# Performance work log

Hardware: AMD Instinct MI355X
Metric: run time of the kernel (lower is better)

## Reference

```python
import jax, jax.numpy as jnp
import numpy as np

N_NODES = 25000
N_EDGES = 500000
ND, ED, G = 32, 19, 200


def _lrelu(x):
    return jax.nn.leaky_relu(x, 0.01)


def setup_inputs() -> dict:
    key = jax.random.key(0)
    ks = jax.random.split(key, 12)
    s = 0.05
    return {
        "node_feats": jax.random.normal(ks[0], (N_NODES, ND), jnp.float32),
        "edge_feats": jax.random.normal(ks[1], (N_EDGES, ED), jnp.float32),
        "src": jax.random.randint(ks[2], (N_EDGES,), 0, N_NODES),
        "dst": jax.random.randint(ks[3], (N_EDGES,), 0, N_NODES),
        "Wn": jax.random.normal(ks[4], (G, ND), jnp.float32) * s,
        "bn": jnp.zeros((G,), jnp.float32),
        "We1": jax.random.normal(ks[5], (G, ND + ED), jnp.float32) * s,
        "be1": jnp.zeros((G,), jnp.float32),
        "We2": jax.random.normal(ks[6], (1, 2 * G), jnp.float32) * s,
        "be2": jnp.zeros((1,), jnp.float32),
        "Wet": jax.random.normal(ks[7], (G, G), jnp.float32) * s,
        "bet": jnp.zeros((G,), jnp.float32),
        "W_ih": jax.random.normal(ks[8], (3 * G, G), jnp.float32) * s,
        "b_ih": jnp.zeros((3 * G,), jnp.float32),
        "W_hh": jax.random.normal(ks[9], (3 * G, G), jnp.float32) * s,
        "b_hh": jnp.zeros((3 * G,), jnp.float32),
    }


def reference(node_feats, edge_feats, src, dst, Wn, bn, We1, be1, We2, be2,
              Wet, bet, W_ih, b_ih, W_hh, b_hh):
    N = node_feats.shape[0]
    # project_node: Linear + LeakyReLU -> hv_new [N, G]
    hv_new = _lrelu(node_feats @ Wn.T + bn)
    # apply_edges1 + project_edge1: cat([src hv, he]) -> he1 [E, G]
    he1 = _lrelu(jnp.concatenate([node_feats[src], edge_feats], axis=1) @ We1.T + be1)
    # apply_edges2 + project_edge2: cat([dst hv_new, he1]) -> logits [E, 1]
    he2 = jnp.concatenate([hv_new[dst], he1], axis=1)
    logits = _lrelu(he2 @ We2.T + be2)[:, 0]  # [E]
    # edge_softmax: softmax over incoming edges per destination node
    m = jax.ops.segment_max(logits, dst, num_segments=N)  # [N]
    ex = jnp.exp(logits - m[dst])
    denom = jax.ops.segment_sum(ex, dst, num_segments=N)  # [N]
    a = ex / denom[dst]  # [E]
    # AttentiveGRU1: e = a * edge_transform(he1); scatter-sum to dst
    e = a[:, None] * (he1 @ Wet.T + bet)  # [E, G]
    c = jax.ops.segment_sum(e, dst, num_segments=N)  # [N, G]
    context = jax.nn.elu(c)
    # GRUCell(context, hv_new)
    gi = context @ W_ih.T + b_ih
    gh = hv_new @ W_hh.T + b_hh
    ir, iz, inn = jnp.split(gi, 3, axis=1)
    hr, hz, hn = jnp.split(gh, 3, axis=1)
    r = jax.nn.sigmoid(ir + hr)
    z = jax.nn.sigmoid(iz + hz)
    n = jnp.tanh(inn + r * hn)
    h = (1.0 - z) * n + z * hv_new
    return jax.nn.relu(h)
```

## Files before the change

### kernel.cpp

```cpp
#include <hip/hip_runtime.h>
#include <hip/hip_bf16.h>

#define G 200
#define NDIM 32
#define EDIM 19
#define KIN 51

typedef unsigned short u16;
typedef unsigned int u32;
typedef unsigned long long u64;

typedef __attribute__((ext_vector_type(8))) short bfrag;
typedef __attribute__((ext_vector_type(4))) float ffrag;

__device__ __forceinline__ float lrelu(float x){ return x > 0.f ? x : 0.01f*x; }
__device__ __forceinline__ u16 f2b(float x){ u32 u = __float_as_uint(x); return (u16)((u + 0x7fffu + ((u >> 16) & 1u)) >> 16); }
__device__ __forceinline__ float b2f(u16 x){ return __uint_as_float(((u32)x) << 16); }

#define MFMA16(a, b, c) __builtin_amdgcn_mfma_f32_16x16x32_bf16(a, b, c, 0, 0, 0)

__global__ void zero_kernel(float* __restrict__ s_raw, float* __restrict__ denom,
                            int* __restrict__ deg, float* __restrict__ l1, int N){
  int i = blockIdx.x * 256 + threadIdx.x;
  if (i < N * G) s_raw[i] = 0.f;
  if (i < N){ denom[i] = 0.f; deg[i] = 0; l1[i] = 0.f; }
}

__global__ void prep_all_kernel(const float* __restrict__ We1, const float* __restrict__ Wn,
                                const float* __restrict__ Wet, const float* __restrict__ Wih,
                                const float* __restrict__ Whh,
                                u16* __restrict__ Wbg, u16* __restrict__ Wnb, u16* __restrict__ Wet2,
                                u16* __restrict__ Wrz, u16* __restrict__ Winn, u16* __restrict__ Whn){
  int idx = blockIdx.x * 256 + threadIdx.x;
  const int s0 = 208 * 64, s1 = 256 * 64, s2 = 208 * 224, s3 = 2 * 208 * 416, s4 = 208 * 224, s5 = 208 * 224;
  if (idx < s0){
    int r = idx >> 6, k = idx & 63;
    Wbg[idx] = f2b((r < G && k < KIN) ? We1[r * KIN + k] : 0.f);
    return;
  }
  idx -= s0;
  if (idx < s1){
    int r = idx >> 6, k = idx & 63;
    Wnb[idx] = f2b((r < G && k < NDIM) ? Wn[r * NDIM + k] : 0.f);
    return;
  }
  idx -= s1;
  if (idx < s2){
    int r = idx / 224, k = idx % 224;
    Wet2[idx] = f2b((r < G && k < G) ? Wet[r * G + k] : 0.f);
    return;
  }
  idx -= s2;
  if (idx < s3){
    int g = idx / (208 * 416), rem = idx % (208 * 416);
    int r = rem / 416, k = rem % 416;
    float v = 0.f;
    if (r < G){
      int row = g * G + r;
      if (k < G) v = Wih[row * G + k];
      else if (k >= 208 && k < 408) v = Whh[row * G + (k - 208)];
    }
    Wrz[idx] = f2b(v);
    return;
  }
  idx -= s3;
  if (idx < s4){
    int r = idx / 224, k = idx % 224;
    Winn[idx] = f2b((r < G && k < G) ? Wih[(2 * G + r) * G + k] : 0.f);
    return;
  }
  idx -= s4;
  if (idx < s5){
    int r = idx / 224, kk = idx % 224;
    Whn[idx] = f2b((r < G && kk >= 16 && kk < 216) ? Whh[(2 * G + r) * G + (kk - 16)] : 0.f);
  }
}

__global__ void deghist_kernel(const int* __restrict__ dst, int* __restrict__ deg, int E){
  int e = blockIdx.x * 256 + threadIdx.x;
  if (e < E) atomicAdd(&deg[dst[e]], 1);
}

__global__ __launch_bounds__(1024) void scan_kernel(const int* __restrict__ deg, int* __restrict__ offs,
                                                    int* __restrict__ cur, int N){
  __shared__ int wsums[16];
  __shared__ int carry_s;
  int tid = threadIdx.x;
  int lane = tid & 63, wid = tid >> 6;
  if (tid == 0) carry_s = 0;
  __syncthreads();
  for (int base = 0; base < N; base += 1024){
    int i = base + tid;
    int v = (i < N) ? deg[i] : 0;
    int x = v;
    #pragma unroll
    for (int off = 1; off < 64; off <<= 1){
      int y = __shfl_up(x, off, 64);
      if (lane >= off) x += y;
    }
    if (lane == 63) wsums[wid] = x;
    __syncthreads();
    if (wid == 0){
      int w = (lane < 16) ? wsums[lane] : 0;
      #pragma unroll
      for (int off = 1; off < 16; off <<= 1){
        int y = __shfl_up(w, off, 64);
        if (lane >= off) w += y;
      }
      if (lane < 16) wsums[lane] = w;
    }
    __syncthreads();
    int wexcl = (wid == 0) ? 0 : wsums[wid - 1];
    int incl = carry_s + wexcl + x;
    if (i < N){ offs[i] = incl - v; cur[i] = incl - v; }
    __syncthreads();
    if (tid == 1023) carry_s = incl;
    __syncthreads();
  }
  if (threadIdx.x == 0) offs[N] = carry_s;
}

__global__ void scatter_kernel(const int* __restrict__ dst, const int* __restrict__ src,
                               int* __restrict__ cur, int* __restrict__ eids,
                               int* __restrict__ dstc, int* __restrict__ srcc, int E){
  int e = blockIdx.x * 256 + threadIdx.x;
  if (e < E){
    int d = dst[e];
    int pos = atomicAdd(&cur[d], 1);
    eids[pos] = e;
    dstc[pos] = d;
    srcc[pos] = src[e];
  }
}

__global__ __launch_bounds__(256) void hvgemm_kernel(
    const float* __restrict__ nf, const u16* __restrict__ Wnb, const float* __restrict__ bn,
    const float* __restrict__ We2, float* __restrict__ hv, float* __restrict__ l1, int M)
{
  __shared__ __align__(16) u16 As[64][72];
  __shared__ __align__(16) u16 Ws[64][72];
  int tid = threadIdx.x;
  int m0 = blockIdx.y * 64, n0 = blockIdx.x * 64;
  int l = tid & 63, w = tid >> 6, quad = l >> 4, col = l & 15;

  for (int idx = tid; idx < 64 * 16; idx += 256){
    int r = idx >> 4, c4 = idx & 15;
    int row = m0 + r, k = c4 * 4;
    float4 v = make_float4(0.f,0.f,0.f,0.f);
    if (row < M && k < NDIM) v = *(const float4*)(nf + (long)row * NDIM + k);
    *(ushort4*)&As[r][c4 * 4] = make_ushort4(f2b(v.x), f2b(v.y), f2b(v.z), f2b(v.w));
  }
  for (int idx = tid; idx < 64 * 8; idx += 256){
    int r = idx >> 3, c = idx & 7;
    *(ulonglong2*)&Ws[r][c * 8] = *(const ulonglong2*)(Wnb + (long)(n0 + r) * 64 + c * 8);
  }
  __syncthreads();
  bfrag a0 = *(const bfrag*)&As[w * 16 + col][quad * 8];
  bfrag a1 = *(const bfrag*)&As[w * 16 + col][32 + quad * 8];
  ffrag acc[4];
  #pragma unroll
  for (int t = 0; t < 4; ++t){ acc[t].x = 0.f; acc[t].y = 0.f; acc[t].z = 0.f; acc[t].w = 0.f; }
  #pragma unroll
  for (int t = 0; t < 4; ++t){
    bfrag b0 = *(const bfrag*)&Ws[t * 16 + col][quad * 8];
    bfrag b1 = *(const bfrag*)&Ws[t * 16 + col][32 + quad * 8];
    acc[t] = MFMA16(a0, b0, acc[t]);
    acc[t] = MFMA16(a1, b1, acc[t]);
  }
  float lp[4] = {0.f, 0.f, 0.f, 0.f};
  #pragma unroll
  for (int t = 0; t < 4; ++t){
    int n = n0 + t * 16 + col;
    float bv = (n < G) ? bn[n] : 0.f;
    float wv = (n < G) ? We2[n] : 0.f;
    #pragma unroll
    for (int r = 0; r < 4; ++r){
      int row = m0 + w * 16 + quad * 4 + r;
      float v = lrelu(acc[t][r] + bv);
      lp[r] += wv * v;
      if (n < G && row < M) hv[(long)row * G + n] = v;
    }
  }
  #pragma unroll
  for (int r = 0; r < 4; ++r){
    lp[r] += __shfl_xor(lp[r], 1, 16);
    lp[r] += __shfl_xor(lp[r], 2, 16);
    lp[r] += __shfl_xor(lp[r], 4, 16);
    lp[r] += __shfl_xor(lp[r], 8, 16);
  }
  if (col == 0){
    #pragma unroll
    for (int r = 0; r < 4; ++r){
      int row = m0 + w * 16 + quad * 4 + r;
      if (row < M) atomicAdd(&l1[row], lp[r]);
    }
  }
}

#define SST 72
__global__ __launch_bounds__(256) void edge_csr_kernel(
    const float* __restrict__ nf, const float* __restrict__ ef,
    const int* __restrict__ eids, const int* __restrict__ dstc, const int* __restrict__ srcc,
    const int* __restrict__ offs,
    const u16* __restrict__ Wbg, const float* __restrict__ be1,
    const float* __restrict__ We2, const float* __restrict__ be2,
    const float* __restrict__ l1,
    float* __restrict__ s_raw, float* __restrict__ denom, int E)
{
  __shared__ __align__(16) u16 shm[208 * SST];
  __shared__ u32 bw_s[208];
  __shared__ int node_s[64], es[64], srcs[64], segnode[64];
  __shared__ __align__(16) u16 exb[64];
  __shared__ __align__(8) unsigned char segb[64];
  __shared__ int Svar;

  int tid = threadIdx.x;
  int j0 = blockIdx.x * 64;

  if (tid < 64){
    int j = j0 + tid;
    int valid = j < E;
    int e = valid ? eids[j] : 0;
    es[tid] = e;
    srcs[tid] = valid ? srcc[j] : 0;
    int n = valid ? dstc[j] : -1;
    node_s[tid] = n;
    int nn = (tid == 63 || j + 1 >= E) ? -2 : dstc[j + 1];
    int f1 = (valid && n != nn) ? 1 : 0;
    int f2 = 0;
    if (f1 && offs[n] >= j0 && offs[n + 1] <= j0 + 64) f2 = 1;
    u64 em = __ballot(f1 != 0);
    int seg = (int)__popcll(em & ((1ull << tid) - 1ull));
    segb[tid] = (unsigned char)seg;
    if (f1) segnode[seg] = (n << 1) | f2;
    if (tid == 0) Svar = (int)__popcll(em);
  }
  if (tid < 208){
    float bv = (tid < G) ? be1[tid] : 0.f;
    float wv = (tid < G) ? We2[G + tid] : 0.f;
    bw_s[tid] = (u32)f2b(bv) | ((u32)f2b(wv) << 16);
  }
  __syncthreads();

  for (int idx = tid; idx < 64 * 8; idx += 256){
    int el = idx >> 3, c = idx & 7;
    float4 v = make_float4(0.f,0.f,0.f,0.f);
    if (j0 + el < E) v = *(const float4*)(nf + (long)srcs[el] * NDIM + c * 4);
    *(ushort4*)&shm[el * SST + c * 4] = make_ushort4(f2b(v.x), f2b(v.y), f2b(v.z), f2b(v.w));
  }
  for (int idx = tid; idx < 64 * EDIM; idx += 256){
    int el = idx / EDIM, k = idx - el * EDIM;
    float v = 0.f;
    if (j0 + el < E) v = ef[(long)es[el] * EDIM + k];
    shm[el * SST + NDIM + k] = f2b(v);
  }
  for (int idx = tid; idx < 64 * 13; idx += 256){
    int el = idx / 13, kk = idx - el * 13;
    shm[el * SST + KIN + kk] = 0;
  }
  __syncthreads();

  int l = tid & 63, w = tid >> 6;
  int quad = l >> 4, col = l & 15;
  int m0 = w * 16;

  bfrag a0 = *(const bfrag*)&shm[(m0 + col) * SST + quad * 8];
  bfrag a1 = *(const bfrag*)&shm[(m0 + col) * SST + 32 + quad * 8];
  __syncthreads();

  if (tid < 64) shm[200 * SST + tid] = 0x3F80;

  float pl[4] = {0.f, 0.f, 0.f, 0.f};
  #pragma unroll
  for (int t = 0; t < 13; ++t){
    bfrag b0 = *(const bfrag*)(Wbg + (t * 16 + col) * 64 + quad * 8);
    bfrag b1 = *(const bfrag*)(Wbg + (t * 16 + col) * 64 + 32 + quad * 8);
    ffrag acc; acc.x = 0.f; acc.y = 0.f; acc.z = 0.f; acc.w = 0.f;
    acc = MFMA16(a0, b0, acc);
    acc = MFMA16(a1, b1, acc);
    int g = t * 16 + col;
    u32 bw = bw_s[g];
    float bv = b2f((u16)(bw & 0xFFFF)), wv = b2f((u16)(bw >> 16));
    float v0 = lrelu(acc.x + bv), v1 = lrelu(acc.y + bv);
    float v2 = lrelu(acc.z + bv), v3 = lrelu(acc.w + bv);
    pl[0] += wv * v0; pl[1] += wv * v1; pl[2] += wv * v2; pl[3] += wv * v3;
    if (g < G)
      *(ushort4*)&shm[g * SST + m0 + quad * 4] = make_ushort4(f2b(v0), f2b(v1), f2b(v2), f2b(v3));
  }
  #pragma unroll
  for (int r = 0; r < 4; ++r){
    pl[r] += __shfl_xor(pl[r], 1, 16);
    pl[r] += __shfl_xor(pl[r], 2, 16);
    pl[r] += __shfl_xor(pl[r], 4, 16);
    pl[r] += __shfl_xor(pl[r], 8, 16);
  }
  if (col == 0){
    #pragma unroll
    for (int r = 0; r < 4; ++r){
      int el = m0 + quad * 4 + r;
      float ex = 0.f;
      if (j0 + el < E){
        int n = node_s[el];
        float lg = lrelu(pl[r] + l1[n] + be2[0]);
        ex = __expf(lg);
      }
      exb[el] = f2b(ex);
    }
  }
  __syncthreads();

  int S = Svar;
  for (int mt = 0; mt * 16 < S; ++mt){
    int m = mt * 16 + col;
    u64 sb0 = *(const u64*)&segb[quad * 8];
    u64 sb1 = *(const u64*)&segb[32 + quad * 8];
    ulonglong2 ew0 = *(const ulonglong2*)&exb[quad * 8];
    ulonglong2 ew1 = *(const ulonglong2*)&exb[32 + quad * 8];
    bfrag A0, A1;
    #pragma unroll
    for (int jj = 0; jj < 8; ++jj){
      int s0i = (int)((sb0 >> (8 * jj)) & 0xFF);
      int s1i = (int)((sb1 >> (8 * jj)) & 0xFF);
      u64 w0 = (jj < 4) ? ew0.x : ew0.y;
      u64 w1 = (jj < 4) ? ew1.x : ew1.y;
      u16 e0 = (u16)(w0 >> (16 * (jj & 3)));
      u16 e1 = (u16)(w1 >> (16 * (jj & 3)));
      A0[jj] = (s0i == m) ? (short)e0 : (short)0;
      A1[jj] = (s1i == m) ? (short)e1 : (short)0;
    }
    int cnt = (w == 3) ? 4 : 3;
    for (int i = 0; i < cnt; ++i){
      int t = w * 3 + i;
      bfrag b0 = *(const bfrag*)&shm[(t * 16 + col) * SST + quad * 8];
      bfrag b1 = *(const bfrag*)&shm[(t * 16 + col) * SST + 32 + quad * 8];
      ffrag acc; acc.x = 0.f; acc.y = 0.f; acc.z = 0.f; acc.w = 0.f;
      acc = MFMA16(A0, b0, acc);
      acc = MFMA16(A1, b1, acc);
      int g = t * 16 + col;
      #pragma unroll
      for (int r = 0; r < 4; ++r){
        int seg = mt * 16 + quad * 4 + r;
        if (seg < S && g <= 200){
          int enc = segnode[seg];
          int nd = enc >> 1;
          float v = acc[r];
          float* pd = (g < G) ? (s_raw + (long)nd * G + g) : (denom + nd);
          if (enc & 1) *pd = v; else atomicAdd(pd, v);
        }
      }
    }
  }
}

__global__ __launch_bounds__(256) void ctxgru_kernel(
    const float* __restrict__ s_raw, const float* __restrict__ hv, const float* __restrict__ denom,
    const u16* __restrict__ Wet2, const u16* __restrict__ Wrz,
    const u16* __restrict__ Winn, const u16* __restrict__ Whn,
    const float* __restrict__ bet, const float* __restrict__ b_ih, const float* __restrict__ b_hh,
    float* __restrict__ out, int M)
{
  __shared__ __align__(16) u16 X[64 * 416];
  __shared__ float invds[64];
  int tid = threadIdx.x;
  int m0 = blockIdx.x * 64;

  if (tid < 64){
    float dn = (m0 + tid < M) ? denom[m0 + tid] : 0.f;
    invds[tid] = dn > 0.f ? 1.f / dn : 0.f;
  }
  __syncthreads();

  for (int idx = tid; idx < 64 * 50; idx += 256){
    int r = idx / 50, c = idx % 50;
    int row = m0 + r;
    float4 v = make_float4(0.f,0.f,0.f,0.f), h = make_float4(0.f,0.f,0.f,0.f);
    if (row < M){
      v = *(const float4*)(s_raw + (long)row * G + c * 4);
      h = *(const float4*)(hv + (long)row * G + c * 4);
    }
    float iv = invds[r];
    *(ushort4*)&X[r * 416 + c * 4] = make_ushort4(f2b(v.x*iv), f2b(v.y*iv), f2b(v.z*iv), f2b(v.w*iv));
    *(ushort4*)&X[r * 416 + 208 + c * 4] = make_ushort4(f2b(h.x), f2b(h.y), f2b(h.z), f2b(h.w));
  }
  for (int idx = tid; idx < 64 * 4; idx += 256){
    int r = idx / 4, q = idx % 4;
    int base = (q < 2) ? (200 + q * 4) : (408 + (q - 2) * 4);
    *(ushort4*)&X[r * 416 + base] = make_ushort4(0,0,0,0);
  }
  __syncthreads();

  int l = tid & 63, w = tid >> 6, quad = l >> 4, col = l & 15;
  int rowbase = w * 16;

  bfrag a1[7];
  #pragma unroll
  for (int j = 0; j < 7; ++j) a1[j] = *(const bfrag*)&X[(rowbase + col) * 416 + j * 32 + quad * 8];

  for (int st = 0; st < 13; ++st){
    int n = st * 16 + col;
    ffrag acc; acc.x = 0.f; acc.y = 0.f; acc.z = 0.f; acc.w = 0.f;
    #pragma unroll
    for (int j = 0; j < 7; ++j){
      bfrag b = *(const bfrag*)(Wet2 + (long)n * 224 + j * 32 + quad * 8);
      acc = MFMA16(a1[j], b, acc);
    }
    if (n < G){
      float bv = bet[n];
      #pragma unroll
      for (int r = 0; r < 4; ++r){
        int lr = rowbase + quad * 4 + r;
        float gate = invds[lr] > 0.f ? 1.f : 0.f;
        float v = acc[r] + gate * bv;
        v = (v > 0.f) ? v : (__expf(v) - 1.f);
        X[lr * 416 + n] = f2b(v);
      }
    }
  }
  __syncthreads();

  bfrag a2[13];
  #pragma unroll
  for (int j = 0; j < 13; ++j) a2[j] = *(const bfrag*)&X[(rowbase + col) * 416 + j * 32 + quad * 8];

  for (int st = 0; st < 13; ++st){
    int n = st * 16 + col;
    ffrag ar, az, ai, ah;
    ar.x=ar.y=ar.z=ar.w=0.f; az.x=az.y=az.z=az.w=0.f;
    ai.x=ai.y=ai.z=ai.w=0.f; ah.x=ah.y=ah.z=ah.w=0.f;
    #pragma unroll
    for (int j = 0; j < 13; ++j){
      bfrag br_ = *(const bfrag*)(Wrz + (long)n * 416 + j * 32 + quad * 8);
      ar = MFMA16(a2[j], br_, ar);
      bfrag bz_ = *(const bfrag*)(Wrz + (long)(208 + n) * 416 + j * 32 + quad * 8);
      az = MFMA16(a2[j], bz_, az);
    }
    #pragma unroll
    for (int j = 0; j < 7; ++j){
      bfrag bi_ = *(const bfrag*)(Winn + (long)n * 224 + j * 32 + quad * 8);
      ai = MFMA16(a2[j], bi_, ai);
      bfrag bh_ = *(const bfrag*)(Whn + (long)n * 224 + j * 32 + quad * 8);
      ah = MFMA16(a2[j + 6], bh_, ah);
    }
    if (n < G){
      float br = b_ih[n] + b_hh[n];
      float bz = b_ih[G + n] + b_hh[G + n];
      float bi = b_ih[2 * G + n];
      float bh = b_hh[2 * G + n];
      #pragma unroll
      for (int r = 0; r < 4; ++r){
        int lr = rowbase + quad * 4 + r;
        int row = m0 + lr;
        if (row < M){
          float rg = 1.f / (1.f + __expf(-(ar[r] + br)));
          float zg = 1.f / (1.f + __expf(-(az[r] + bz)));
          float ng = tanhf(ai[r] + bi + rg * (ah[r] + bh));
          float hvv = b2f(X[lr * 416 + 208 + n]);
          float h = (1.f - zg) * ng + zg * hvv;
          out[(long)row * G + n] = h > 0.f ? h : 0.f;
        }
      }
    }
  }
}

extern "C" void kernel_launch(void* const* d_in, const int* in_sizes, int n_in,
                              void* d_out, int out_size, void* d_ws, size_t ws_size,
                              hipStream_t stream)
{
  const float* nf   = (const float*)d_in[0];
  const float* ef   = (const float*)d_in[1];
  const int*   src  = (const int*)d_in[2];
  const int*   dst  = (const int*)d_in[3];
  const float* Wn   = (const float*)d_in[4];
  const float* bn   = (const float*)d_in[5];
  const float* We1  = (const float*)d_in[6];
  const float* be1  = (const float*)d_in[7];
  const float* We2  = (const float*)d_in[8];
  const float* be2  = (const float*)d_in[9];
  const float* Wet  = (const float*)d_in[10];
  const float* bet  = (const float*)d_in[11];
  const float* W_ih = (const float*)d_in[12];
  const float* b_ih = (const float*)d_in[13];
  const float* W_hh = (const float*)d_in[14];
  const float* b_hh = (const float*)d_in[15];
  int N = in_sizes[0] / NDIM;
  int E = in_sizes[2];
  float* out = (float*)d_out;

  char* p = (char*)d_ws;
  auto alloc = [&](size_t b){ char* r = p; p += (b + 255) & ~(size_t)255; return r; };
  float* hv    = (float*)alloc((size_t)N * G * 4);
  float* s_raw = (float*)alloc((size_t)N * G * 4);
  float* denom = (float*)alloc((size_t)N * 4);
  int*   deg   = (int*)  alloc((size_t)N * 4);
  int*   offs  = (int*)  alloc((size_t)(N + 1) * 4);
  int*   cur   = (int*)  alloc((size_t)N * 4);
  int*   eids  = (int*)  alloc((size_t)E * 4);
  int*   dstc  = (int*)  alloc((size_t)E * 4);
  int*   srcc  = (int*)  alloc((size_t)E * 4);
  float* l1    = (float*)alloc((size_t)N * 4);
  u16*   Wbg   = (u16*)  alloc((size_t)208 * 64 * 2);
  u16*   Wnb   = (u16*)  alloc((size_t)256 * 64 * 2);
  u16*   Wet2  = (u16*)  alloc((size_t)208 * 224 * 2);
  u16*   Wrz   = (u16*)  alloc((size_t)2 * 208 * 416 * 2);
  u16*   Winn  = (u16*)  alloc((size_t)208 * 224 * 2);
  u16*   Whn   = (u16*)  alloc((size_t)208 * 224 * 2);

  int eb = (E + 255) / 256;
  int mb = (N + 63) / 64;
  const int prep_total = 208*64 + 256*64 + 208*224 + 2*208*416 + 208*224 + 208*224;

  zero_kernel<<<dim3((N * G + 255) / 256), dim3(256), 0, stream>>>(s_raw, denom, deg, l1, N);
  prep_all_kernel<<<dim3((prep_total + 255) / 256), dim3(256), 0, stream>>>(
      We1, Wn, Wet, W_ih, W_hh, Wbg, Wnb, Wet2, Wrz, Winn, Whn);
  deghist_kernel<<<dim3(eb), dim3(256), 0, stream>>>(dst, deg, E);
  scan_kernel<<<dim3(1), dim3(1024), 0, stream>>>(deg, offs, cur, N);
  scatter_kernel<<<dim3(eb), dim3(256), 0, stream>>>(dst, src, cur, eids, dstc, srcc, E);
  hvgemm_kernel<<<dim3(4, mb), dim3(256), 0, stream>>>(nf, Wnb, bn, We2, hv, l1, N);
  edge_csr_kernel<<<dim3((E + 63) / 64), dim3(256), 0, stream>>>(nf, ef, eids, dstc, srcc, offs,
                                                                 Wbg, be1, We2, be2, l1, s_raw, denom, E);
  ctxgru_kernel<<<dim3(mb), dim3(256), 0, stream>>>(s_raw, hv, denom, Wet2, Wrz, Winn, Whn,
                                                    bet, b_ih, b_hh, out, N);
}
```

Before: 458.8 us.

## Pack edge data in CSR order as bf16, single-pass scan, pad GRU smem stride

After: 435.7 us. 1.05x faster.

```diff
diff --git a/kernel.cpp b/kernel.cpp
--- a/kernel.cpp
+++ b/kernel.cpp
@@ -20,10 +20,12 @@
 #define MFMA16(a, b, c) __builtin_amdgcn_mfma_f32_16x16x32_bf16(a, b, c, 0, 0, 0)
 
 __global__ void zero_kernel(float* __restrict__ s_raw, float* __restrict__ denom,
-                            int* __restrict__ deg, float* __restrict__ l1, int N){
+                            int* __restrict__ deg, float* __restrict__ l1,
+                            const float* __restrict__ nf, u16* __restrict__ nfb, int N){
   int i = blockIdx.x * 256 + threadIdx.x;
   if (i < N * G) s_raw[i] = 0.f;
   if (i < N){ denom[i] = 0.f; deg[i] = 0; l1[i] = 0.f; }
+  if (i < N * NDIM) nfb[i] = f2b(nf[i]);
 }
 
 __global__ void prep_all_kernel(const float* __restrict__ We1, const float* __restrict__ Wn,
@@ -84,53 +86,66 @@
 __global__ __launch_bounds__(1024) void scan_kernel(const int* __restrict__ deg, int* __restrict__ offs,
                                                     int* __restrict__ cur, int N){
   __shared__ int wsums[16];
-  __shared__ int carry_s;
+  const int C = 25;
   int tid = threadIdx.x;
   int lane = tid & 63, wid = tid >> 6;
-  if (tid == 0) carry_s = 0;
-  __syncthreads();
-  for (int base = 0; base < N; base += 1024){
-    int i = base + tid;
-    int v = (i < N) ? deg[i] : 0;
-    int x = v;
-    #pragma unroll
-    for (int off = 1; off < 64; off <<= 1){
-      int y = __shfl_up(x, off, 64);
-      if (lane >= off) x += y;
-    }
-    if (lane == 63) wsums[wid] = x;
-    __syncthreads();
-    if (wid == 0){
-      int w = (lane < 16) ? wsums[lane] : 0;
-      #pragma unroll
-      for (int off = 1; off < 16; off <<= 1){
-        int y = __shfl_up(w, off, 64);
-        if (lane >= off) w += y;
-      }
-      if (lane < 16) wsums[lane] = w;
-    }
-    __syncthreads();
-    int wexcl = (wid == 0) ? 0 : wsums[wid - 1];
-    int incl = carry_s + wexcl + x;
-    if (i < N){ offs[i] = incl - v; cur[i] = incl - v; }
-    __syncthreads();
-    if (tid == 1023) carry_s = incl;
-    __syncthreads();
-  }
-  if (threadIdx.x == 0) offs[N] = carry_s;
-}
-
-__global__ void scatter_kernel(const int* __restrict__ dst, const int* __restrict__ src,
-                               int* __restrict__ cur, int* __restrict__ eids,
-                               int* __restrict__ dstc, int* __restrict__ srcc, int E){
+  int base = tid * C;
+  int loc[C];
+  int s = 0;
+  #pragma unroll
+  for (int i = 0; i < C; ++i){
+    int v = (base + i < N) ? deg[base + i] : 0;
+    loc[i] = s; s += v;
+  }
+  int x = s;
+  #pragma unroll
+  for (int off = 1; off < 64; off <<= 1){
+    int y = __shfl_up(x, off, 64);
+    if (lane >= off) x += y;
+  }
+  if (lane == 63) wsums[wid] = x;
+  __syncthreads();
+  if (wid == 0){
+    int w = (lane < 16) ? wsums[lane] : 0;
+    #pragma unroll
+    for (int off = 1; off < 16; off <<= 1){
+      int y = __shfl_up(w, off, 64);
+      if (lane >= off) w += y;
+    }
+    if (lane < 16) wsums[lane] = w;
+  }
+  __syncthreads();
+  int excl = ((wid ? wsums[wid - 1] : 0) + x) - s;
+  #pragma unroll
+  for (int i = 0; i < C; ++i){
+    int o = excl + loc[i];
+    if (base + i < N){ offs[base + i] = o; cur[base + i] = o; }
+  }
+  if (tid == 1023) offs[N] = excl + s;
+}
+
+__global__ void scatter_pack_kernel(const int* __restrict__ dst, const int* __restrict__ src,
+                                    const float* __restrict__ ef,
+                                    int* __restrict__ cur, int2* __restrict__ ds2,
+                                    u16* __restrict__ efc, int E){
   int e = blockIdx.x * 256 + threadIdx.x;
-  if (e < E){
-    int d = dst[e];
-    int pos = atomicAdd(&cur[d], 1);
-    eids[pos] = e;
-    dstc[pos] = d;
-    srcc[pos] = src[e];
-  }
+  if (e >= E) return;
+  int d = dst[e];
+  int pos = atomicAdd(&cur[d], 1);
+  ds2[pos] = make_int2(d, src[e]);
+  const float* ep = ef + (long)e * EDIM;
+  u32 w[12];
+  #pragma unroll
+  for (int j = 0; j < 12; ++j){
+    int k0 = 2 * j, k1 = 2 * j + 1;
+    u16 lo = (k0 < EDIM) ? f2b(ep[k0]) : (u16)0;
+    u16 hi = (k1 < EDIM) ? f2b(ep[k1]) : (u16)0;
+    w[j] = (u32)lo | ((u32)hi << 16);
+  }
+  uint4* dp = (uint4*)(efc + (long)pos * 24);
+  dp[0] = make_uint4(w[0], w[1], w[2], w[3]);
+  dp[1] = make_uint4(w[4], w[5], w[6], w[7]);
+  dp[2] = make_uint4(w[8], w[9], w[10], w[11]);
 }
 
 __global__ __launch_bounds__(256) void hvgemm_kernel(
@@ -199,9 +214,8 @@
 
 #define SST 72
 __global__ __launch_bounds__(256) void edge_csr_kernel(
-    const float* __restrict__ nf, const float* __restrict__ ef,
-    const int* __restrict__ eids, const int* __restrict__ dstc, const int* __restrict__ srcc,
-    const int* __restrict__ offs,
+    const u16* __restrict__ nfb, const u16* __restrict__ efc,
+    const int2* __restrict__ ds2, const int* __restrict__ offs,
     const u16* __restrict__ Wbg, const float* __restrict__ be1,
     const float* __restrict__ We2, const float* __restrict__ be2,
     const float* __restrict__ l1,
@@ -209,7 +223,7 @@
 {
   __shared__ __align__(16) u16 shm[208 * SST];
   __shared__ u32 bw_s[208];
-  __shared__ int node_s[64], es[64], srcs[64], segnode[64];
+  __shared__ int node_s[64], srcs[64], segnode[64];
   __shared__ __align__(16) u16 exb[64];
   __shared__ __align__(8) unsigned char segb[64];
   __shared__ int Svar;
@@ -220,12 +234,11 @@
   if (tid < 64){
     int j = j0 + tid;
     int valid = j < E;
-    int e = valid ? eids[j] : 0;
-    es[tid] = e;
-    srcs[tid] = valid ? srcc[j] : 0;
-    int n = valid ? dstc[j] : -1;
+    int2 p = valid ? ds2[j] : make_int2(-1, 0);
+    srcs[tid] = p.y;
+    int n = valid ? p.x : -1;
     node_s[tid] = n;
-    int nn = (tid == 63 || j + 1 >= E) ? -2 : dstc[j + 1];
+    int nn = (tid == 63 || j + 1 >= E) ? -2 : ds2[j + 1].x;
     int f1 = (valid && n != nn) ? 1 : 0;
     int f2 = 0;
     if (f1 && offs[n] >= j0 && offs[n + 1] <= j0 + 64) f2 = 1;
@@ -242,22 +255,19 @@
   }
   __syncthreads();
 
-  for (int idx = tid; idx < 64 * 8; idx += 256){
-    int el = idx >> 3, c = idx & 7;
-    float4 v = make_float4(0.f,0.f,0.f,0.f);
-    if (j0 + el < E) v = *(const float4*)(nf + (long)srcs[el] * NDIM + c * 4);
-    *(ushort4*)&shm[el * SST + c * 4] = make_ushort4(f2b(v.x), f2b(v.y), f2b(v.z), f2b(v.w));
-  }
-  for (int idx = tid; idx < 64 * EDIM; idx += 256){
-    int el = idx / EDIM, k = idx - el * EDIM;
-    float v = 0.f;
-    if (j0 + el < E) v = ef[(long)es[el] * EDIM + k];
-    shm[el * SST + NDIM + k] = f2b(v);
-  }
-  for (int idx = tid; idx < 64 * 13; idx += 256){
-    int el = idx / 13, kk = idx - el * 13;
-    shm[el * SST + KIN + kk] = 0;
-  }
+  for (int idx = tid; idx < 64 * 4; idx += 256){
+    int el = idx >> 2, c = idx & 3;
+    ulonglong2 v; v.x = 0; v.y = 0;
+    if (j0 + el < E) v = *(const ulonglong2*)(nfb + (long)srcs[el] * NDIM + c * 8);
+    *(ulonglong2*)&shm[el * SST + c * 8] = v;
+  }
+  for (int idx = tid; idx < 64 * 3; idx += 256){
+    int el = idx / 3, c = idx - el * 3;
+    ulonglong2 v; v.x = 0; v.y = 0;
+    if (j0 + el < E) v = *(const ulonglong2*)(efc + (long)(j0 + el) * 24 + c * 8);
+    *(ulonglong2*)&shm[el * SST + NDIM + c * 8] = v;
+  }
+  if (tid < 64){ ulonglong2 z; z.x = 0; z.y = 0; *(ulonglong2*)&shm[tid * SST + 56] = z; }
   __syncthreads();
 
   int l = tid & 63, w = tid >> 6;
@@ -352,6 +362,7 @@
   }
 }
 
+#define XST 420
 __global__ __launch_bounds__(256) void ctxgru_kernel(
     const float* __restrict__ s_raw, const float* __restrict__ hv, const float* __restrict__ denom,
     const u16* __restrict__ Wet2, const u16* __restrict__ Wrz,
@@ -359,7 +370,7 @@
     const float* __restrict__ bet, const float* __restrict__ b_ih, const float* __restrict__ b_hh,
     float* __restrict__ out, int M)
 {
-  __shared__ __align__(16) u16 X[64 * 416];
+  __shared__ __align__(16) u16 X[64 * XST];
   __shared__ float invds[64];
   int tid = threadIdx.x;
   int m0 = blockIdx.x * 64;
@@ -379,13 +390,13 @@
       h = *(const float4*)(hv + (long)row * G + c * 4);
     }
     float iv = invds[r];
-    *(ushort4*)&X[r * 416 + c * 4] = make_ushort4(f2b(v.x*iv), f2b(v.y*iv), f2b(v.z*iv), f2b(v.w*iv));
-    *(ushort4*)&X[r * 416 + 208 + c * 4] = make_ushort4(f2b(h.x), f2b(h.y), f2b(h.z), f2b(h.w));
+    *(ushort4*)&X[r * XST + c * 4] = make_ushort4(f2b(v.x*iv), f2b(v.y*iv), f2b(v.z*iv), f2b(v.w*iv));
+    *(ushort4*)&X[r * XST + 208 + c * 4] = make_ushort4(f2b(h.x), f2b(h.y), f2b(h.z), f2b(h.w));
   }
   for (int idx = tid; idx < 64 * 4; idx += 256){
     int r = idx / 4, q = idx % 4;
     int base = (q < 2) ? (200 + q * 4) : (408 + (q - 2) * 4);
-    *(ushort4*)&X[r * 416 + base] = make_ushort4(0,0,0,0);
+    *(ushort4*)&X[r * XST + base] = make_ushort4(0,0,0,0);
   }
   __syncthreads();
 
@@ -394,7 +405,7 @@
 
   bfrag a1[7];
   #pragma unroll
-  for (int j = 0; j < 7; ++j) a1[j] = *(const bfrag*)&X[(rowbase + col) * 416 + j * 32 + quad * 8];
+  for (int j = 0; j < 7; ++j) a1[j] = *(const bfrag*)&X[(rowbase + col) * XST + j * 32 + quad * 8];
 
   for (int st = 0; st < 13; ++st){
     int n = st * 16 + col;
@@ -412,7 +423,7 @@
         float gate = invds[lr] > 0.f ? 1.f : 0.f;
         float v = acc[r] + gate * bv;
         v = (v > 0.f) ? v : (__expf(v) - 1.f);
-        X[lr * 416 + n] = f2b(v);
+        X[lr * XST + n] = f2b(v);
       }
     }
   }
@@ -420,7 +431,7 @@
 
   bfrag a2[13];
   #pragma unroll
-  for (int j = 0; j < 13; ++j) a2[j] = *(const bfrag*)&X[(rowbase + col) * 416 + j * 32 + quad * 8];
+  for (int j = 0; j < 13; ++j) a2[j] = *(const bfrag*)&X[(rowbase + col) * XST + j * 32 + quad * 8];
 
   for (int st = 0; st < 13; ++st){
     int n = st * 16 + col;
@@ -454,7 +465,7 @@
           float rg = 1.f / (1.f + __expf(-(ar[r] + br)));
           float zg = 1.f / (1.f + __expf(-(az[r] + bz)));
           float ng = tanhf(ai[r] + bi + rg * (ah[r] + bh));
-          float hvv = b2f(X[lr * 416 + 208 + n]);
+          float hvv = b2f(X[lr * XST + 208 + n]);
           float h = (1.f - zg) * ng + zg * hvv;
           out[(long)row * G + n] = h > 0.f ? h : 0.f;
         }
@@ -495,9 +506,9 @@
   int*   deg   = (int*)  alloc((size_t)N * 4);
   int*   offs  = (int*)  alloc((size_t)(N + 1) * 4);
   int*   cur   = (int*)  alloc((size_t)N * 4);
-  int*   eids  = (int*)  alloc((size_t)E * 4);
-  int*   dstc  = (int*)  alloc((size_t)E * 4);
-  int*   srcc  = (int*)  alloc((size_t)E * 4);
+  int2*  ds2   = (int2*) alloc((size_t)E * 8);
+  u16*   efc   = (u16*)  alloc((size_t)E * 24 * 2);
+  u16*   nfb   = (u16*)  alloc((size_t)N * NDIM * 2);
   float* l1    = (float*)alloc((size_t)N * 4);
   u16*   Wbg   = (u16*)  alloc((size_t)208 * 64 * 2);
   u16*   Wnb   = (u16*)  alloc((size_t)256 * 64 * 2);
@@ -510,14 +521,14 @@
   int mb = (N + 63) / 64;
   const int prep_total = 208*64 + 256*64 + 208*224 + 2*208*416 + 208*224 + 208*224;
 
-  zero_kernel<<<dim3((N * G + 255) / 256), dim3(256), 0, stream>>>(s_raw, denom, deg, l1, N);
+  zero_kernel<<<dim3((N * G + 255) / 256), dim3(256), 0, stream>>>(s_raw, denom, deg, l1, nf, nfb, N);
   prep_all_kernel<<<dim3((prep_total + 255) / 256), dim3(256), 0, stream>>>(
       We1, Wn, Wet, W_ih, W_hh, Wbg, Wnb, Wet2, Wrz, Winn, Whn);
   deghist_kernel<<<dim3(eb), dim3(256), 0, stream>>>(dst, deg, E);
   scan_kernel<<<dim3(1), dim3(1024), 0, stream>>>(deg, offs, cur, N);
-  scatter_kernel<<<dim3(eb), dim3(256), 0, stream>>>(dst, src, cur, eids, dstc, srcc, E);
+  scatter_pack_kernel<<<dim3(eb), dim3(256), 0, stream>>>(dst, src, ef, cur, ds2, efc, E);
   hvgemm_kernel<<<dim3(4, mb), dim3(256), 0, stream>>>(nf, Wnb, bn, We2, hv, l1, N);
-  edge_csr_kernel<<<dim3((E + 63) / 64), dim3(256), 0, stream>>>(nf, ef, eids, dstc, srcc, offs,
+  edge_csr_kernel<<<dim3((E + 63) / 64), dim3(256), 0, stream>>>(nfb, efc, ds2, offs,
                                                                  Wbg, be1, We2, be2, l1, s_raw, denom, E);
   ctxgru_kernel<<<dim3(mb), dim3(256), 0, stream>>>(s_raw, hv, denom, Wet2, Wrz, Winn, Whn,
                                                     bet, b_ih, b_hh, out, N);
```
